# Optimization experiments

Hardware: AMD Instinct MI355X
Metric: run time of the kernel (lower is better)

Reference implementation:

```python
import jax, jax.numpy as jnp
import numpy as np

NUM_ITERATIONS = 3


def _squash_elementwise(s):
    # Faithful to original: squared_norm summed over trailing axis of size 1
    # => elementwise squash v = s^2 * s / ((1 + s^2) * sqrt(s^2))
    sq = s * s
    return sq * s / ((1.0 + sq) * jnp.sqrt(sq))


def setup_inputs() -> dict:
    key = jax.random.key(0)
    k1, k2 = jax.random.split(key)
    B, R, C, O, I = 256, 1152, 10, 16, 8
    x = jax.random.normal(k1, (B, R, I), dtype=jnp.float32)
    W = jax.random.normal(k2, (R, C, O, I), dtype=jnp.float32)
    return {"x": x, "W": W}


def reference(x, W):
    # x: (B, R, I); W: (R, C, O, I)
    R, C, O, I = W.shape
    # u_hat[b,r,c,o] = sum_i W[r,c,o,i] * x[b,r,i]   (matmul W @ x per route/capsule)
    u_hat = jnp.einsum('rcoi,bri->brco', W, x)  # (B, R, C, O)
    b_ij = jnp.zeros((R, C), dtype=x.dtype)  # batch-shared routing logits
    v = None
    for it in range(NUM_ITERATIONS):
        c_ij = jax.nn.softmax(b_ij, axis=0)  # softmax over routes (dim=1 in torch)
        s_j = jnp.einsum('rc,brco->bco', c_ij, u_hat)  # weighted sum over routes
        v = _squash_elementwise(s_j)  # (B, C, O)
        if it < NUM_ITERATIONS - 1:
            # agreement a[b,r,c] = u_hat[b,r,c,:] . v[b,c,:]
            a_ij = jnp.einsum('brco,bco->brc', u_hat, v)
            b_ij = b_ij + a_ij.mean(axis=0)  # mean over batch, batch-shared update
    return v[..., None]  # (B, C, O, 1) matches v_j.squeeze(1)
```

## Files before the change

kernel.cpp:

```cpp
#include <hip/hip_runtime.h>

static constexpr int B_ = 256;
static constexpr int R_ = 1152;
static constexpr int C_ = 10;
static constexpr int O_ = 16;
static constexpr int I_ = 8;
static constexpr int SCO = C_ * O_;
static constexpr int K_ = R_ * I_;

typedef short bf16x8 __attribute__((ext_vector_type(8)));
typedef float f32x4  __attribute__((ext_vector_type(4)));

__device__ __forceinline__ unsigned short f2bf(float f) {
  union { float f; unsigned int u; } c; c.f = f;
  const unsigned int u = c.u;
  return (unsigned short)((u + 0x7fffu + ((u >> 16) & 1u)) >> 16);
}
__device__ __forceinline__ float bf2f(unsigned short h) {
  union { unsigned int u; float f; } c; c.u = ((unsigned int)h) << 16; return c.f;
}

__global__ __launch_bounds__(256) void prep0(const float* __restrict__ x,
                                             const float* __restrict__ W,
                                             unsigned short* __restrict__ xb,
                                             unsigned short* __restrict__ wraw,
                                             unsigned short* __restrict__ xT,
                                             float* __restrict__ sbuf,
                                             unsigned int* __restrict__ cnt,
                                             float* __restrict__ Z) {
  const int bx = blockIdx.x;
  const int t  = threadIdx.x;
  const int zi = bx * 256 + t;
  if (zi < 3 * 160 * 256) sbuf[zi] = 0.0f;
  if (zi < 512) cnt[zi] = 0u;
  if (zi < 32)  Z[zi] = (zi < 10) ? 1152.0f : 0.0f;
  if (bx < 256) {
    const float4* wf = (const float4*)W;
    ushort4* wr = (ushort4*)wraw;
    for (int idx = bx * 256 + t; idx < (R_ * C_ * O_ * I_) / 4; idx += 65536) {
      const float4 v4 = wf[idx];
      ushort4 r4;
      r4.x = f2bf(v4.x); r4.y = f2bf(v4.y); r4.z = f2bf(v4.z); r4.w = f2bf(v4.w);
      wr[idx] = r4;
    }
  } else {
    __shared__ float sx[18 * 8 * 68];
    const int idx2 = bx - 256;
    const int bq = idx2 & 3, rseg = idx2 >> 2;
    const int rbase = rseg * 18;
    for (int idx = t; idx < 64 * 36; idx += 256) {
      const int b = idx / 36, f4 = idx - b * 36;
      const size_t off = (size_t)(bq * 64 + b) * K_ + rbase * I_ + f4 * 4;
      const float4 val = *(const float4*)(x + off);
      ushort4 o4;
      o4.x = f2bf(val.x); o4.y = f2bf(val.y); o4.z = f2bf(val.z); o4.w = f2bf(val.w);
      *(ushort4*)(xb + off) = o4;
      const int rr = f4 >> 1, i4 = (f4 & 1) * 4;
      sx[(rr * 8 + i4 + 0) * 68 + b] = val.x;
      sx[(rr * 8 + i4 + 1) * 68 + b] = val.y;
      sx[(rr * 8 + i4 + 2) * 68 + b] = val.z;
      sx[(rr * 8 + i4 + 3) * 68 + b] = val.w;
    }
    __syncthreads();
    const int lane = t & 63, w = t >> 6;
    for (int row = w * 36; row < w * 36 + 36; ++row)
      xT[(size_t)(rbase * 8 + row) * 256 + bq * 64 + lane] = f2bf(sx[row * 68 + lane]);
  }
}

__global__ __launch_bounds__(512) void k_gemm(const unsigned short* __restrict__ xb,
                                              const unsigned short* __restrict__ Bm,
                                              const float* __restrict__ Zit,
                                              unsigned short* __restrict__ vb,
                                              float* __restrict__ out,
                                              float* __restrict__ sbuf,
                                              unsigned int* __restrict__ cnt,
                                              int final_) {
  __shared__ float sred[8][16 * 17];
  __shared__ int sflag;
  const int bx = blockIdx.x;
  const int g = (bx & 7) * 40 + (bx >> 3);
  const int mtile = g / 20;
  const int rem = g - mtile * 20;
  const int c = rem >> 1, sub = rem & 1;
  const int t = threadIdx.x, lane = t & 63;
  const int w = __builtin_amdgcn_readfirstlane(t >> 6);
  const int mrow = lane & 15, quad = lane >> 4;
  const int m0 = mtile * 16;
  const int kb = sub * 4608 + w * 576;
  const int rb = sub * 576 + w * 72;

  const unsigned short* ap = xb + (size_t)(m0 + mrow) * K_ + kb + quad * 8;
  const unsigned short* bp = Bm + ((size_t)(rb + quad) * C_ + c) * 128 + mrow * 8;
  f32x4 acc = {0.0f, 0.0f, 0.0f, 0.0f};
#pragma unroll 6
  for (int kk = 0; kk < 18; ++kk) {
    const bf16x8 a = *(const bf16x8*)(ap + kk * 32);
    const bf16x8 b = *(const bf16x8*)(bp + (size_t)kk * 4 * C_ * 128);
    acc = __builtin_amdgcn_mfma_f32_16x16x32_bf16(a, b, acc, 0, 0, 0);
  }
#pragma unroll
  for (int rg = 0; rg < 4; ++rg)
    sred[w][mrow * 17 + quad * 4 + rg] = acc[rg];
  __syncthreads();
  const int tile = mtile * 10 + c;
  int m = 0, n = 0;
  if (t < 256) {
    if (final_) { m = t >> 4; n = t & 15; } else { n = t >> 4; m = t & 15; }
    const int e = n * 17 + m;
    const float val = ((sred[0][e] + sred[1][e]) + (sred[2][e] + sred[3][e]))
                    + ((sred[4][e] + sred[5][e]) + (sred[6][e] + sred[7][e]));
    atomicAdd(&sbuf[(size_t)tile * 256 + t], val);
  }
  __syncthreads();
  if (t == 0) sflag = (int)atomicAdd(&cnt[tile], 1u);
  __syncthreads();
  if (sflag == 0) return;
  if (t < 256) {
    const float tot = atomicAdd(&sbuf[(size_t)tile * 256 + t], 0.0f);
    const float s = tot / Zit[c];
    const float v = s * fabsf(s) / (1.0f + s * s);
    if (final_) out[(size_t)(m0 + m) * SCO + c * 16 + n] = v;
    else        vb[(size_t)(c * 16 + n) * 256 + m0 + m] = f2bf(v);
  }
}

__global__ __launch_bounds__(256) void k_pv(const unsigned short* __restrict__ xT,
                                            const unsigned short* __restrict__ vb,
                                            const float* __restrict__ W,
                                            const unsigned short* __restrict__ wraw,
                                            unsigned short* __restrict__ wb2,
                                            float* __restrict__ bvec,
                                            float* __restrict__ Zout,
                                            int first) {
  __shared__ __align__(16) unsigned short svb[40960];
  __shared__ float sbs[80];
  const int bx = blockIdx.x;
  const int seg = (bx & 7) * 18 + (bx >> 3);
  const int r0 = seg * 8;
  const int t = threadIdx.x, lane = t & 63;
  const int w = __builtin_amdgcn_readfirstlane(t >> 6);
  const int mrow = lane & 15, quad = lane >> 4;

  const unsigned short* ap = xT + (size_t)(seg * 64 + w * 16 + mrow) * 256 + quad * 8;
  bf16x8 afr[8];
#pragma unroll
  for (int kk = 0; kk < 8; ++kk) afr[kk] = *(const bf16x8*)(ap + kk * 32);

  {
    const char* src = (const char*)vb;
    char* dst = (char*)svb;
#pragma unroll
    for (int i = 0; i < 20; ++i) {
      const int ci = i * 256 + t;
      const int lin = ci * 16;
      const int n = ci >> 5;
      *(bf16x8*)(dst + (lin ^ ((n & 7) << 4))) = *(const bf16x8*)(src + lin);
    }
  }
  __syncthreads();

  f32x4 acc[10];
#pragma unroll
  for (int c = 0; c < 10; ++c) acc[c] = (f32x4){0.0f, 0.0f, 0.0f, 0.0f};
#pragma unroll
  for (int c = 0; c < 10; ++c) {
    const int n = c * 16 + mrow;
    const int base = n * 512 + quad * 16;
#pragma unroll
    for (int kk = 0; kk < 8; ++kk) {
      const bf16x8 b = *(const bf16x8*)((const char*)svb +
                        ((base + kk * 64) ^ ((n & 7) << 4)));
      acc[c] = __builtin_amdgcn_mfma_f32_16x16x32_bf16(afr[kk], b, acc[c], 0, 0, 0);
    }
  }
  __syncthreads();

  float* sp = (float*)svb;
#pragma unroll
  for (int c = 0; c < 10; ++c)
#pragma unroll
    for (int rg = 0; rg < 4; ++rg) {
      const int ml = w * 16 + quad * 4 + rg;
      sp[(c * 8 + (ml >> 3)) * 128 + mrow * 8 + (ml & 7)] = acc[c][rg];
    }
  __syncthreads();

  const int p8 = t >> 5, l32 = t & 31;
#pragma unroll
  for (int ch = 0; ch < 10; ++ch) {
    const int pair = ch * 8 + p8;
    const int rl = pair / 10, c = pair - rl * 10;
    const float4 pv = *(const float4*)&sp[(c * 8 + rl) * 128 + l32 * 4];
    const float4 wv = *(const float4*)(W + (size_t)(r0 + rl) * 1280 + c * 128 + l32 * 4);
    float prod = wv.x * pv.x + wv.y * pv.y + wv.z * pv.z + wv.w * pv.w;
    prod += __shfl_xor(prod, 1);  prod += __shfl_xor(prod, 2);
    prod += __shfl_xor(prod, 4);  prod += __shfl_xor(prod, 8);
    prod += __shfl_xor(prod, 16);
    if (l32 == 0) sbs[rl * 10 + c] = prod;
  }
  __syncthreads();

  if (t < 80) {
    const int rl = t / 10, c = t - rl * 10;
    const int r = r0 + rl;
    float b = sbs[t] * (1.0f / 256.0f);
    if (!first) b += bvec[r * C_ + c];
    bvec[r * C_ + c] = b;
    sbs[t] = expf(b);
  }
  __syncthreads();
  if (t < 10) {
    float z = 0.0f;
#pragma unroll
    for (int rl = 0; rl < 8; ++rl) z += sbs[rl * 10 + t];
    atomicAdd(&Zout[t], z);
  }

#pragma unroll
  for (int i = 0; i < 5; ++i) {
    const int base = i * 2048 + t * 8;
    const int rl = base / 1280, rem2 = base - rl * 1280;
    const int c = rem2 >> 7;
    const float e = sbs[rl * 10 + c];
    const size_t off = ((size_t)(r0 + rl) * C_ + c) * 128 + (rem2 & 127);
    const bf16x8 wv8 = *(const bf16x8*)(wraw + off);
    bf16x8 o8;
#pragma unroll
    for (int j = 0; j < 8; ++j)
      o8[j] = (short)f2bf(bf2f((unsigned short)wv8[j]) * e);
    *(bf16x8*)(wb2 + off) = o8;
  }
}

extern "C" void kernel_launch(void* const* d_in, const int* in_sizes, int n_in,
                              void* d_out, int out_size, void* d_ws, size_t ws_size,
                              hipStream_t stream) {
  const float* x = (const float*)d_in[0];
  const float* W = (const float*)d_in[1];
  float* out = (float*)d_out;

  float* bvec = (float*)d_ws;
  float* Z    = bvec + R_ * C_;
  float* sbuf = Z + 32;
  unsigned int* cnt = (unsigned int*)(sbuf + 3 * 160 * 256);
  unsigned short* xb   = (unsigned short*)(cnt + 512);
  unsigned short* wraw = xb + (size_t)B_ * K_;
  unsigned short* xT   = wraw + (size_t)R_ * C_ * O_ * I_;
  unsigned short* vb   = xT + (size_t)R_ * 8 * 256;
  unsigned short* wb2  = vb + (size_t)160 * 256;

  prep0<<<512, 256, 0, stream>>>(x, W, xb, wraw, xT, sbuf, cnt, Z);
  k_gemm<<<320, 512, 0, stream>>>(xb, wraw, Z + 0,  vb, out, sbuf + 0 * 40960, cnt + 0,   0);
  k_pv  <<<144, 256, 0, stream>>>(xT, vb, W, wraw, wb2, bvec, Z + 10, 1);
  k_gemm<<<320, 512, 0, stream>>>(xb, wb2,  Z + 10, vb, out, sbuf + 1 * 40960, cnt + 160, 0);
  k_pv  <<<144, 256, 0, stream>>>(xT, vb, W, wraw, wb2, bvec, Z + 20, 0);
  k_gemm<<<320, 512, 0, stream>>>(xb, wb2,  Z + 20, vb, out, sbuf + 2 * 40960, cnt + 320, 1);
}
```

Measured before the change: 131.1 us.

## Fuse all routing stages into one persistent kernel with grid barriers

Replaces the six separate launches (prep, three GEMMs, two agreement kernels) with a single persistent kernel of 160 blocks that steps through the stages, separated by atomic-counter grid barriers. The GEMM no longer splits K across two blocks with atomic accumulation and a last-arriver counter. Each block now reduces the full K range itself, and the agreement stage uses 72 blocks of 16 routes each. The aim is to remove launch gaps and atomic reduction traffic, at the cost of fewer blocks in flight, idle blocks during the agreement phase, and spin-wait barrier overhead that relies on all blocks being co-resident.

```diff
diff --git a/kernel.cpp b/kernel.cpp
--- a/kernel.cpp
+++ b/kernel.cpp
@@ -7,6 +7,7 @@
 static constexpr int I_ = 8;
 static constexpr int SCO = C_ * O_;
 static constexpr int K_ = R_ * I_;
+static constexpr int NB = 160;
 
 typedef short bf16x8 __attribute__((ext_vector_type(8)));
 typedef float f32x4  __attribute__((ext_vector_type(4)));
@@ -20,216 +21,205 @@
   union { unsigned int u; float f; } c; c.u = ((unsigned int)h) << 16; return c.f;
 }
 
-__global__ __launch_bounds__(256) void prep0(const float* __restrict__ x,
-                                             const float* __restrict__ W,
-                                             unsigned short* __restrict__ xb,
-                                             unsigned short* __restrict__ wraw,
-                                             unsigned short* __restrict__ xT,
-                                             float* __restrict__ sbuf,
-                                             unsigned int* __restrict__ cnt,
-                                             float* __restrict__ Z) {
+__device__ __forceinline__ void gsync(unsigned int* bar, unsigned int target) {
+  __syncthreads();
+  if (threadIdx.x == 0) {
+    __hip_atomic_fetch_add(bar, 1u, __ATOMIC_ACQ_REL, __HIP_MEMORY_SCOPE_AGENT);
+    int guard = 0;
+    while (__hip_atomic_load(bar, __ATOMIC_ACQUIRE, __HIP_MEMORY_SCOPE_AGENT) < target) {
+      __builtin_amdgcn_s_sleep(2);
+      if (++guard > (1 << 22)) break;
+    }
+  }
+  __syncthreads();
+}
+
+__global__ __launch_bounds__(512, 1) void mega(
+    const float* __restrict__ x, const float* __restrict__ W,
+    float* __restrict__ out, unsigned int* __restrict__ bar,
+    float* __restrict__ bvec, float* __restrict__ Z,
+    unsigned short* __restrict__ xb, unsigned short* __restrict__ wraw,
+    unsigned short* __restrict__ xT,
+    unsigned short* __restrict__ vb0, unsigned short* __restrict__ vb1,
+    unsigned short* __restrict__ wb2a, unsigned short* __restrict__ wb2b) {
+  __shared__ __align__(16) unsigned char smem[82560];
   const int bx = blockIdx.x;
-  const int t  = threadIdx.x;
-  const int zi = bx * 256 + t;
-  if (zi < 3 * 160 * 256) sbuf[zi] = 0.0f;
-  if (zi < 512) cnt[zi] = 0u;
-  if (zi < 32)  Z[zi] = (zi < 10) ? 1152.0f : 0.0f;
-  if (bx < 256) {
+  const int t = threadIdx.x;
+  const int lane = t & 63;
+  const int w = __builtin_amdgcn_readfirstlane(t >> 6);
+  const int mrow = lane & 15, quad = lane >> 4;
+
+  {
     const float4* wf = (const float4*)W;
     ushort4* wr = (ushort4*)wraw;
-    for (int idx = bx * 256 + t; idx < (R_ * C_ * O_ * I_) / 4; idx += 65536) {
-      const float4 v4 = wf[idx];
+    for (int idx = t; idx < 2304; idx += 512) {
+      const int j = bx * 2304 + idx;
+      const float4 v4 = wf[j];
       ushort4 r4;
       r4.x = f2bf(v4.x); r4.y = f2bf(v4.y); r4.z = f2bf(v4.z); r4.w = f2bf(v4.w);
-      wr[idx] = r4;
-    }
-  } else {
-    __shared__ float sx[18 * 8 * 68];
-    const int idx2 = bx - 256;
-    const int bq = idx2 & 3, rseg = idx2 >> 2;
-    const int rbase = rseg * 18;
-    for (int idx = t; idx < 64 * 36; idx += 256) {
-      const int b = idx / 36, f4 = idx - b * 36;
-      const size_t off = (size_t)(bq * 64 + b) * K_ + rbase * I_ + f4 * 4;
-      const float4 val = *(const float4*)(x + off);
-      ushort4 o4;
-      o4.x = f2bf(val.x); o4.y = f2bf(val.y); o4.z = f2bf(val.z); o4.w = f2bf(val.w);
-      *(ushort4*)(xb + off) = o4;
-      const int rr = f4 >> 1, i4 = (f4 & 1) * 4;
-      sx[(rr * 8 + i4 + 0) * 68 + b] = val.x;
-      sx[(rr * 8 + i4 + 1) * 68 + b] = val.y;
-      sx[(rr * 8 + i4 + 2) * 68 + b] = val.z;
-      sx[(rr * 8 + i4 + 3) * 68 + b] = val.w;
-    }
-    __syncthreads();
-    const int lane = t & 63, w = t >> 6;
-    for (int row = w * 36; row < w * 36 + 36; ++row)
-      xT[(size_t)(rbase * 8 + row) * 256 + bq * 64 + lane] = f2bf(sx[row * 68 + lane]);
+      wr[j] = r4;
+    }
+    if (bx == 0 && t < 32) Z[t] = 0.0f;
+    float* sx = (float*)smem;
+    for (int u = bx; u < 256; u += NB) {
+      const int bq = u & 3, rseg = u >> 2;
+      const int rbase = rseg * 18;
+      __syncthreads();
+      for (int idx = t; idx < 64 * 36; idx += 512) {
+        const int b = idx / 36, f4 = idx - b * 36;
+        const size_t off = (size_t)(bq * 64 + b) * K_ + rbase * I_ + f4 * 4;
+        const float4 val = *(const float4*)(x + off);
+        ushort4 o4;
+        o4.x = f2bf(val.x); o4.y = f2bf(val.y); o4.z = f2bf(val.z); o4.w = f2bf(val.w);
+        *(ushort4*)(xb + off) = o4;
+        const int rr = f4 >> 1, i4 = (f4 & 1) * 4;
+        sx[(rr * 8 + i4 + 0) * 68 + b] = val.x;
+        sx[(rr * 8 + i4 + 1) * 68 + b] = val.y;
+        sx[(rr * 8 + i4 + 2) * 68 + b] = val.z;
+        sx[(rr * 8 + i4 + 3) * 68 + b] = val.w;
+      }
+      __syncthreads();
+      for (int row = w * 18; row < w * 18 + 18; ++row)
+        xT[(size_t)(rseg * 144 + row) * 256 + bq * 64 + lane] = f2bf(sx[row * 68 + lane]);
+    }
   }
-}
-
-__global__ __launch_bounds__(512) void k_gemm(const unsigned short* __restrict__ xb,
-                                              const unsigned short* __restrict__ Bm,
-                                              const float* __restrict__ Zit,
-                                              unsigned short* __restrict__ vb,
-                                              float* __restrict__ out,
-                                              float* __restrict__ sbuf,
-                                              unsigned int* __restrict__ cnt,
-                                              int final_) {
-  __shared__ float sred[8][16 * 17];
-  __shared__ int sflag;
-  const int bx = blockIdx.x;
-  const int g = (bx & 7) * 40 + (bx >> 3);
-  const int mtile = g / 20;
-  const int rem = g - mtile * 20;
-  const int c = rem >> 1, sub = rem & 1;
-  const int t = threadIdx.x, lane = t & 63;
-  const int w = __builtin_amdgcn_readfirstlane(t >> 6);
-  const int mrow = lane & 15, quad = lane >> 4;
-  const int m0 = mtile * 16;
-  const int kb = sub * 4608 + w * 576;
-  const int rb = sub * 576 + w * 72;
-
-  const unsigned short* ap = xb + (size_t)(m0 + mrow) * K_ + kb + quad * 8;
-  const unsigned short* bp = Bm + ((size_t)(rb + quad) * C_ + c) * 128 + mrow * 8;
-  f32x4 acc = {0.0f, 0.0f, 0.0f, 0.0f};
+  gsync(bar, NB);
+
+  for (int it = 0; it < 3; ++it) {
+    {
+      float* sred = (float*)smem;
+      float* szed = (float*)(smem + 16384);
+      const unsigned short* Bm = (it == 0) ? wraw : (it == 1 ? wb2a : wb2b);
+      const int g = (bx & 7) * 20 + (bx >> 3);
+      const int mtile = g / 10, c = g - mtile * 10;
+      const int m0 = mtile * 16;
+      const unsigned short* ap = xb + (size_t)(m0 + mrow) * K_ + w * 1152 + quad * 8;
+      const unsigned short* bp = Bm + ((size_t)(w * 144 + quad) * C_ + c) * 128 + mrow * 8;
+      if (t < 10) szed[t] = (it == 0) ? 1152.0f
+                                      : atomicAdd(&Z[it * 10 + t], 0.0f);
+      f32x4 acc = {0.0f, 0.0f, 0.0f, 0.0f};
 #pragma unroll 6
-  for (int kk = 0; kk < 18; ++kk) {
-    const bf16x8 a = *(const bf16x8*)(ap + kk * 32);
-    const bf16x8 b = *(const bf16x8*)(bp + (size_t)kk * 4 * C_ * 128);
-    acc = __builtin_amdgcn_mfma_f32_16x16x32_bf16(a, b, acc, 0, 0, 0);
-  }
-#pragma unroll
-  for (int rg = 0; rg < 4; ++rg)
-    sred[w][mrow * 17 + quad * 4 + rg] = acc[rg];
-  __syncthreads();
-  const int tile = mtile * 10 + c;
-  int m = 0, n = 0;
-  if (t < 256) {
-    if (final_) { m = t >> 4; n = t & 15; } else { n = t >> 4; m = t & 15; }
-    const int e = n * 17 + m;
-    const float val = ((sred[0][e] + sred[1][e]) + (sred[2][e] + sred[3][e]))
-                    + ((sred[4][e] + sred[5][e]) + (sred[6][e] + sred[7][e]));
-    atomicAdd(&sbuf[(size_t)tile * 256 + t], val);
-  }
-  __syncthreads();
-  if (t == 0) sflag = (int)atomicAdd(&cnt[tile], 1u);
-  __syncthreads();
-  if (sflag == 0) return;
-  if (t < 256) {
-    const float tot = atomicAdd(&sbuf[(size_t)tile * 256 + t], 0.0f);
-    const float s = tot / Zit[c];
-    const float v = s * fabsf(s) / (1.0f + s * s);
-    if (final_) out[(size_t)(m0 + m) * SCO + c * 16 + n] = v;
-    else        vb[(size_t)(c * 16 + n) * 256 + m0 + m] = f2bf(v);
-  }
-}
-
-__global__ __launch_bounds__(256) void k_pv(const unsigned short* __restrict__ xT,
-                                            const unsigned short* __restrict__ vb,
-                                            const float* __restrict__ W,
-                                            const unsigned short* __restrict__ wraw,
-                                            unsigned short* __restrict__ wb2,
-                                            float* __restrict__ bvec,
-                                            float* __restrict__ Zout,
-                                            int first) {
-  __shared__ __align__(16) unsigned short svb[40960];
-  __shared__ float sbs[80];
-  const int bx = blockIdx.x;
-  const int seg = (bx & 7) * 18 + (bx >> 3);
-  const int r0 = seg * 8;
-  const int t = threadIdx.x, lane = t & 63;
-  const int w = __builtin_amdgcn_readfirstlane(t >> 6);
-  const int mrow = lane & 15, quad = lane >> 4;
-
-  const unsigned short* ap = xT + (size_t)(seg * 64 + w * 16 + mrow) * 256 + quad * 8;
-  bf16x8 afr[8];
-#pragma unroll
-  for (int kk = 0; kk < 8; ++kk) afr[kk] = *(const bf16x8*)(ap + kk * 32);
-
-  {
-    const char* src = (const char*)vb;
-    char* dst = (char*)svb;
-#pragma unroll
-    for (int i = 0; i < 20; ++i) {
-      const int ci = i * 256 + t;
-      const int lin = ci * 16;
-      const int n = ci >> 5;
-      *(bf16x8*)(dst + (lin ^ ((n & 7) << 4))) = *(const bf16x8*)(src + lin);
-    }
-  }
-  __syncthreads();
-
-  f32x4 acc[10];
-#pragma unroll
-  for (int c = 0; c < 10; ++c) acc[c] = (f32x4){0.0f, 0.0f, 0.0f, 0.0f};
-#pragma unroll
-  for (int c = 0; c < 10; ++c) {
-    const int n = c * 16 + mrow;
-    const int base = n * 512 + quad * 16;
-#pragma unroll
-    for (int kk = 0; kk < 8; ++kk) {
-      const bf16x8 b = *(const bf16x8*)((const char*)svb +
-                        ((base + kk * 64) ^ ((n & 7) << 4)));
-      acc[c] = __builtin_amdgcn_mfma_f32_16x16x32_bf16(afr[kk], b, acc[c], 0, 0, 0);
-    }
-  }
-  __syncthreads();
-
-  float* sp = (float*)svb;
-#pragma unroll
-  for (int c = 0; c < 10; ++c)
-#pragma unroll
-    for (int rg = 0; rg < 4; ++rg) {
-      const int ml = w * 16 + quad * 4 + rg;
-      sp[(c * 8 + (ml >> 3)) * 128 + mrow * 8 + (ml & 7)] = acc[c][rg];
-    }
-  __syncthreads();
-
-  const int p8 = t >> 5, l32 = t & 31;
-#pragma unroll
-  for (int ch = 0; ch < 10; ++ch) {
-    const int pair = ch * 8 + p8;
-    const int rl = pair / 10, c = pair - rl * 10;
-    const float4 pv = *(const float4*)&sp[(c * 8 + rl) * 128 + l32 * 4];
-    const float4 wv = *(const float4*)(W + (size_t)(r0 + rl) * 1280 + c * 128 + l32 * 4);
-    float prod = wv.x * pv.x + wv.y * pv.y + wv.z * pv.z + wv.w * pv.w;
-    prod += __shfl_xor(prod, 1);  prod += __shfl_xor(prod, 2);
-    prod += __shfl_xor(prod, 4);  prod += __shfl_xor(prod, 8);
-    prod += __shfl_xor(prod, 16);
-    if (l32 == 0) sbs[rl * 10 + c] = prod;
-  }
-  __syncthreads();
-
-  if (t < 80) {
-    const int rl = t / 10, c = t - rl * 10;
-    const int r = r0 + rl;
-    float b = sbs[t] * (1.0f / 256.0f);
-    if (!first) b += bvec[r * C_ + c];
-    bvec[r * C_ + c] = b;
-    sbs[t] = expf(b);
-  }
-  __syncthreads();
-  if (t < 10) {
-    float z = 0.0f;
-#pragma unroll
-    for (int rl = 0; rl < 8; ++rl) z += sbs[rl * 10 + t];
-    atomicAdd(&Zout[t], z);
-  }
-
-#pragma unroll
-  for (int i = 0; i < 5; ++i) {
-    const int base = i * 2048 + t * 8;
-    const int rl = base / 1280, rem2 = base - rl * 1280;
-    const int c = rem2 >> 7;
-    const float e = sbs[rl * 10 + c];
-    const size_t off = ((size_t)(r0 + rl) * C_ + c) * 128 + (rem2 & 127);
-    const bf16x8 wv8 = *(const bf16x8*)(wraw + off);
-    bf16x8 o8;
-#pragma unroll
-    for (int j = 0; j < 8; ++j)
-      o8[j] = (short)f2bf(bf2f((unsigned short)wv8[j]) * e);
-    *(bf16x8*)(wb2 + off) = o8;
+      for (int kk = 0; kk < 36; ++kk) {
+        const bf16x8 a = *(const bf16x8*)(ap + kk * 32);
+        const bf16x8 b = *(const bf16x8*)(bp + (size_t)kk * 5120);
+        acc = __builtin_amdgcn_mfma_f32_16x16x32_bf16(a, b, acc, 0, 0, 0);
+      }
+#pragma unroll
+      for (int rg = 0; rg < 4; ++rg)
+        sred[w * 272 + mrow * 17 + quad * 4 + rg] = acc[rg];
+      __syncthreads();
+      if (t < 256) {
+        int m, n;
+        if (it == 2) { m = t >> 4; n = t & 15; } else { n = t >> 4; m = t & 15; }
+        const int e = n * 17 + m;
+        const float ss = ((sred[0 * 272 + e] + sred[1 * 272 + e]) +
+                          (sred[2 * 272 + e] + sred[3 * 272 + e])) +
+                         ((sred[4 * 272 + e] + sred[5 * 272 + e]) +
+                          (sred[6 * 272 + e] + sred[7 * 272 + e]));
+        const float s = ss / szed[c];
+        const float v = s * fabsf(s) / (1.0f + s * s);
+        if (it == 2) out[(size_t)(m0 + m) * SCO + c * 16 + n] = v;
+        else {
+          unsigned short* vbw = (it == 0) ? vb0 : vb1;
+          vbw[(size_t)(c * 16 + n) * 256 + m0 + m] = f2bf(v);
+        }
+      }
+    }
+    if (it == 2) break;
+    gsync(bar, (unsigned)NB * (2 * it + 2));
+
+    if (bx < 72) {
+      unsigned short* svb = (unsigned short*)smem;
+      float* sp = (float*)smem;
+      float* sbs = (float*)(smem + 81920);
+      const unsigned short* vbr = (it == 0) ? vb0 : vb1;
+      unsigned short* wb2w = (it == 0) ? wb2a : wb2b;
+      const int seg = (bx & 7) * 9 + (bx >> 3);
+      const int r0 = seg * 16;
+      const unsigned short* ap = xT + (size_t)(seg * 128 + w * 16 + mrow) * 256 + quad * 8;
+      bf16x8 afr[8];
+#pragma unroll
+      for (int kk = 0; kk < 8; ++kk) afr[kk] = *(const bf16x8*)(ap + kk * 32);
+      {
+        const char* src = (const char*)vbr;
+        char* dst = (char*)svb;
+#pragma unroll
+        for (int i = 0; i < 10; ++i) {
+          const int ci = i * 512 + t;
+          const int lin = ci * 16;
+          const int n = ci >> 5;
+          *(bf16x8*)(dst + (lin ^ ((n & 7) << 4))) = *(const bf16x8*)(src + lin);
+        }
+      }
+      __syncthreads();
+      f32x4 acc[10];
+#pragma unroll
+      for (int c = 0; c < 10; ++c) acc[c] = (f32x4){0.0f, 0.0f, 0.0f, 0.0f};
+#pragma unroll
+      for (int c = 0; c < 10; ++c) {
+        const int n = c * 16 + mrow;
+        const int base = n * 512 + quad * 16;
+#pragma unroll
+        for (int kk = 0; kk < 8; ++kk) {
+          const bf16x8 b = *(const bf16x8*)((const char*)svb +
+                            ((base + kk * 64) ^ ((n & 7) << 4)));
+          acc[c] = __builtin_amdgcn_mfma_f32_16x16x32_bf16(afr[kk], b, acc[c], 0, 0, 0);
+        }
+      }
+      __syncthreads();
+#pragma unroll
+      for (int c = 0; c < 10; ++c)
+#pragma unroll
+        for (int rg = 0; rg < 4; ++rg) {
+          const int ml = w * 16 + quad * 4 + rg;
+          sp[(c * 16 + (ml >> 3)) * 128 + mrow * 8 + (ml & 7)] = acc[c][rg];
+        }
+      __syncthreads();
+      const int p16 = t >> 5, l32 = t & 31;
+#pragma unroll
+      for (int ch = 0; ch < 10; ++ch) {
+        const int pair = ch * 16 + p16;
+        const int rl = pair / 10, c = pair - rl * 10;
+        const float4 pv = *(const float4*)&sp[(c * 16 + rl) * 128 + l32 * 4];
+        const float4 wv = *(const float4*)(W + (size_t)(r0 + rl) * 1280 + c * 128 + l32 * 4);
+        float prod = wv.x * pv.x + wv.y * pv.y + wv.z * pv.z + wv.w * pv.w;
+        prod += __shfl_xor(prod, 1);  prod += __shfl_xor(prod, 2);
+        prod += __shfl_xor(prod, 4);  prod += __shfl_xor(prod, 8);
+        prod += __shfl_xor(prod, 16);
+        if (l32 == 0) sbs[rl * 10 + c] = prod;
+      }
+      __syncthreads();
+      if (t < 160) {
+        const int rl = t / 10, c = t - rl * 10;
+        const int r = r0 + rl;
+        float b = sbs[t] * (1.0f / 256.0f);
+        if (it != 0) b += bvec[r * C_ + c];
+        bvec[r * C_ + c] = b;
+        sbs[t] = expf(b);
+      }
+      __syncthreads();
+      if (t < 10) {
+        float z = 0.0f;
+#pragma unroll
+        for (int rl = 0; rl < 16; ++rl) z += sbs[rl * 10 + t];
+        atomicAdd(&Z[(it + 1) * 10 + t], z);
+      }
+#pragma unroll
+      for (int i = 0; i < 5; ++i) {
+        const int base = i * 4096 + t * 8;
+        const int rl = base / 1280, rem2 = base - rl * 1280;
+        const int c = rem2 >> 7;
+        const float e = sbs[rl * 10 + c];
+        const size_t off = ((size_t)(r0 + rl) * C_ + c) * 128 + (rem2 & 127);
+        const bf16x8 wv8 = *(const bf16x8*)(wraw + off);
+        bf16x8 o8;
+#pragma unroll
+        for (int j = 0; j < 8; ++j)
+          o8[j] = (short)f2bf(bf2f((unsigned short)wv8[j]) * e);
+        *(bf16x8*)(wb2w + off) = o8;
+      }
+    }
+    gsync(bar, (unsigned)NB * (2 * it + 3));
   }
 }
 
@@ -240,20 +230,18 @@
   const float* W = (const float*)d_in[1];
   float* out = (float*)d_out;
 
-  float* bvec = (float*)d_ws;
+  unsigned int* bar = (unsigned int*)d_ws;
+  float* bvec = (float*)d_ws + 16;
   float* Z    = bvec + R_ * C_;
-  float* sbuf = Z + 32;
-  unsigned int* cnt = (unsigned int*)(sbuf + 3 * 160 * 256);
-  unsigned short* xb   = (unsigned short*)(cnt + 512);
+  unsigned short* xb   = (unsigned short*)(Z + 32);
   unsigned short* wraw = xb + (size_t)B_ * K_;
   unsigned short* xT   = wraw + (size_t)R_ * C_ * O_ * I_;
-  unsigned short* vb   = xT + (size_t)R_ * 8 * 256;
-  unsigned short* wb2  = vb + (size_t)160 * 256;
-
-  prep0<<<512, 256, 0, stream>>>(x, W, xb, wraw, xT, sbuf, cnt, Z);
-  k_gemm<<<320, 512, 0, stream>>>(xb, wraw, Z + 0,  vb, out, sbuf + 0 * 40960, cnt + 0,   0);
-  k_pv  <<<144, 256, 0, stream>>>(xT, vb, W, wraw, wb2, bvec, Z + 10, 1);
-  k_gemm<<<320, 512, 0, stream>>>(xb, wb2,  Z + 10, vb, out, sbuf + 1 * 40960, cnt + 160, 0);
-  k_pv  <<<144, 256, 0, stream>>>(xT, vb, W, wraw, wb2, bvec, Z + 20, 0);
-  k_gemm<<<320, 512, 0, stream>>>(xb, wb2,  Z + 20, vb, out, sbuf + 2 * 40960, cnt + 320, 1);
-}
+  unsigned short* vb0  = xT + (size_t)R_ * 8 * 256;
+  unsigned short* vb1  = vb0 + (size_t)160 * 256;
+  unsigned short* wb2a = vb1 + (size_t)160 * 256;
+  unsigned short* wb2b = wb2a + (size_t)R_ * C_ * O_ * I_;
+
+  hipMemsetAsync(bar, 0, 64, stream);
+  mega<<<NB, 512, 0, stream>>>(x, W, out, bar, bvec, Z, xb, wraw, xT,
+                               vb0, vb1, wb2a, wb2b);
+}
```

New measurement: 206.8 us. 1.58x slower.
